# Kernel tuning notes

Measured on AMD Instinct MI355X. Metric: run time of the kernel, lower is better.

Reference implementation:

```python
import jax, jax.numpy as jnp
import numpy as np
import math

B, T, D, H, DFF = 4, 1024, 1024, 16, 4096
HD = D // H

def _c(a):
    # a: float array [2, ...] -> complex64 (a[0] real, a[1] imag)
    return jax.lax.complex(a[0], a[1])

def _clinear(z, W, b):
    # complex y = z @ W^T + b (torch nn.Linear convention)
    return z @ _c(W).T + _c(b)

def _cln(z, g, b, eps=1e-5):
    # per-component LayerNorm with separate affine for real/imag parts
    def ln(r):
        m = r.mean(-1, keepdims=True)
        v = ((r - m) ** 2).mean(-1, keepdims=True)
        return (r - m) / jnp.sqrt(v + eps)
    return jax.lax.complex(ln(z.real) * g[0] + b[0], ln(z.imag) * g[1] + b[1])

def _rope_phasor(t_len, dim):
    inv_freq = 1.0 / (10000.0 ** (jnp.arange(dim, dtype=jnp.float32) / dim))
    freqs = jnp.arange(t_len, dtype=jnp.float32)[:, None] * inv_freq[None, :]
    return jax.lax.complex(jnp.cos(freqs), jnp.sin(freqs))  # [T, HD]


def setup_inputs():
    key = jax.random.key(0)
    ks = iter(jax.random.split(key, 40))
    def p(shape, scale=0.02):
        return jax.random.normal(next(ks), shape, jnp.float32) * scale
    inp = {"x": p((2, B, T, D), 1.0), "mask": jnp.tril(jnp.ones((T, T), bool))}
    dims = {"wq": (D, D), "wk": (D, D), "wv": (D, D), "wo": (D, D),
            "wf1": (DFF, D), "wf2": (D, DFF), "wg": (D, D)}
    for name, (o, i) in dims.items():
        inp[name] = p((2, o, i))
        inp["b" + name[1:]] = p((2, o))
    inp["g1"] = jnp.ones((2, D), jnp.float32)
    inp["b1"] = jnp.zeros((2, D), jnp.float32)
    inp["g2"] = jnp.ones((2, D), jnp.float32)
    inp["b2"] = jnp.zeros((2, D), jnp.float32)
    return inp


def reference(x, mask, wq, bq, wk, bk, wv, bv, wo, bo,
              wf1, bf1, wf2, bf2, wg, bg, g1, b1, g2, b2):
    z = _c(x)  # [B,T,D] complex64
    ph = _rope_phasor(T, HD)[None, None]  # [1,1,T,HD]

    # ---- attention branch (pre-norm) ----
    nz = _cln(z, g1, b1)
    heads = lambda t: t.reshape(B, T, H, HD).transpose(0, 2, 1, 3)  # [B,H,T,HD]
    q = heads(_clinear(nz, wq, bq)) * ph
    k = heads(_clinear(nz, wk, bk)) * ph
    v = heads(_clinear(nz, wv, bv))
    score = jnp.einsum('bhqd,bhkd->bhqk', q, jnp.conj(k)) / math.sqrt(HD)
    mag = jnp.where(mask, jnp.abs(score), jnp.float32(-1e9))
    aw = jax.nn.softmax(mag, axis=-1)
    awc = jax.lax.complex(aw, jnp.zeros_like(aw))
    o = jnp.einsum('bhqk,bhkd->bhqd', awc, v)
    o = o.transpose(0, 2, 1, 3).reshape(B, T, D)
    z = z + _clinear(o, wo, bo)

    # ---- FFN branch with CReLU and AntiMatterGate ----
    nz = _cln(z, g2, b2)
    h = _clinear(nz, wf1, bf1)
    h = jax.lax.complex(jax.nn.relu(h.real), jax.nn.relu(h.imag))  # CReLU
    h = _clinear(h, wf2, bf2)
    g = _clinear(h, wg, bg)
    gn = jnp.abs(g) + 1e-8
    h = h * (g / jax.lax.complex(gn, jnp.zeros_like(gn)))  # phase-only gate
    z = z + h
    return jnp.stack([z.real, z.imag], axis=0)  # [2,B,T,D] float32
```

## Files before the change

### kernel.cpp

```cpp
#include <hip/hip_runtime.h>
#include <math.h>

#define B_ 4
#define T_ 1024
#define D_ 1024
#define H_ 16
#define DFF_ 4096
#define HD_ 64
#define BT_ (B_*T_)
#define PL ((size_t)BT_*D_)

typedef unsigned int uint;
typedef unsigned short ushort;
typedef __attribute__((ext_vector_type(8))) __bf16 bf16x8;
typedef __attribute__((ext_vector_type(4))) float f32x4;
typedef __attribute__((ext_vector_type(4))) uint uint4v;

__device__ __forceinline__ float b2f(ushort u){
  union{uint i; float f;} x; x.i = ((uint)u)<<16; return x.f;
}
__device__ __forceinline__ ushort f2b(float f){
  union{float f; uint i;} x; x.f = f;
  uint r = x.i + 0x7fffu + ((x.i>>16)&1u);
  return (ushort)(r>>16);
}
__device__ __forceinline__ void fsplit(float x, ushort& hi, ushort& lo){
  hi = f2b(x);
  lo = f2b(x - b2f(hi));
}
__device__ __forceinline__ bf16x8 negv(bf16x8 v){
  union{bf16x8 b; uint4v u;} t; t.b = v;
  t.u ^= 0x80008000u;
  return t.b;
}
__device__ __forceinline__ f32x4 mfma16(bf16x8 a, bf16x8 b, f32x4 c){
  return __builtin_amdgcn_mfma_f32_16x16x32_bf16(a,b,c,0,0,0);
}
__device__ __forceinline__ float block_sum(float v, float* sm){
  #pragma unroll
  for (int o=32;o>0;o>>=1) v += __shfl_down(v,o);
  int wid = threadIdx.x>>6;
  if ((threadIdx.x&63)==0) sm[wid]=v;
  __syncthreads();
  float r = sm[0]+sm[1]+sm[2]+sm[3];
  __syncthreads();
  return r;
}

__global__ __launch_bounds__(256) void cvt_split(const float* __restrict__ s,
                                                 ushort* __restrict__ d, long NK){
  long i = ((long)blockIdx.x*256 + threadIdx.x)*4;
  if (i >= NK) return;
  float4 vr = *(const float4*)(s+i);
  float4 vi = *(const float4*)(s+NK+i);
  ushort4 rh, rl, ih4, il4;
  fsplit(vr.x, rh.x, rl.x); fsplit(vr.y, rh.y, rl.y);
  fsplit(vr.z, rh.z, rl.z); fsplit(vr.w, rh.w, rl.w);
  fsplit(vi.x, ih4.x, il4.x); fsplit(vi.y, ih4.y, il4.y);
  fsplit(vi.z, ih4.z, il4.z); fsplit(vi.w, ih4.w, il4.w);
  *(ushort4*)(d + i)        = rh;
  *(ushort4*)(d + NK + i)   = rl;
  *(ushort4*)(d + 2*NK + i) = ih4;
  *(ushort4*)(d + 3*NK + i) = il4;
}

__global__ __launch_bounds__(256) void cln_kernel(const float* __restrict__ x,
    long PSx, int row0, const float* __restrict__ g, const float* __restrict__ bb,
    ushort* __restrict__ out, long PSo)
{
  __shared__ float sm[4];
  int row = blockIdx.x, comp = blockIdx.y;
  const float* xr = x + (size_t)comp*PSx + (size_t)(row0+row)*D_;
  float4 v = *(const float4*)(xr + threadIdx.x*4);
  float s = v.x+v.y+v.z+v.w;
  s = block_sum(s, sm);
  float mean = s * (1.0f/D_);
  float dx=v.x-mean, dy=v.y-mean, dz=v.z-mean, dw=v.w-mean;
  float s2 = dx*dx+dy*dy+dz*dz+dw*dw;
  s2 = block_sum(s2, sm);
  float inv = 1.0f/sqrtf(s2*(1.0f/D_) + 1e-5f);
  float4 gv = *(const float4*)(g + comp*D_ + threadIdx.x*4);
  float4 bv = *(const float4*)(bb + comp*D_ + threadIdx.x*4);
  float y0 = dx*inv*gv.x + bv.x, y1 = dy*inv*gv.y + bv.y;
  float y2 = dz*inv*gv.z + bv.z, y3 = dw*inv*gv.w + bv.w;
  ushort4 hh, ll;
  fsplit(y0, hh.x, ll.x); fsplit(y1, hh.y, ll.y);
  fsplit(y2, hh.z, ll.z); fsplit(y3, hh.w, ll.w);
  ushort* oh = out + (size_t)(comp*2)*PSo   + (size_t)row*D_;
  ushort* ol = out + (size_t)(comp*2+1)*PSo + (size_t)row*D_;
  *(ushort4*)(oh + threadIdx.x*4) = hh;
  *(ushort4*)(ol + threadIdx.x*4) = ll;
}

template<int BM,int BN,int WM,int WN,int NT>
__global__ __launch_bounds__(NT,1) void cgemm_split(
    const ushort* __restrict__ A, long PSa,
    const ushort* __restrict__ W, long PSw, long wstride,
    const float* b0, const float* b1, const float* b2,
    const float* __restrict__ Rr, const float* __restrict__ Ri,
    float* __restrict__ Cf, long PSc, long ostrideF,
    ushort* __restrict__ Cs, long PSs, long ostrideS,
    int M, int N, int K, int relu, int biasRow, int kslice)
{
  constexpr int NI = WM/16, NJ = WN/16;
  constexpr int NWX = BN/WN;
  constexpr int NPW = (BM+BN)*16/NT;
  constexpr int BUF = (BM+BN)*128;
  __shared__ __align__(16) ushort lds[2*BUF];
  const int tid = threadIdx.x, wave = tid>>6, lane = tid&63;
  const int quad = lane>>4, l16 = lane&15;
  const int lrow = lane>>3, sl = lane&7;

  const int gx = gridDim.x, gy = gridDim.y;
  const int nt = gx*gy;
  int lin = blockIdx.x + gx*blockIdx.y;
  int tile = (nt&7) ? lin : ((lin&7)*(nt>>3) + (lin>>3));
  int bxi, byi;
  if (gx <= gy){ bxi = tile % gx; byi = tile / gx; }
  else         { byi = tile % gy; bxi = tile / gy; }
  const int bm = byi*BM, bn = bxi*BN;

  const int gz = blockIdx.z;
  W += (size_t)gz*wstride;
  const float* bias = (gz==0)? b0 : (gz==1)? b1 : b2;
  if (Cf) Cf += (size_t)gz*ostrideF;
  if (Cs) Cs += (size_t)gz*ostrideS;
  const int wm = (wave/NWX)*WM, wn = (wave%NWX)*WN;
  const int kbeg = kslice ? gz*kslice : 0;
  const int kend = kslice ? kbeg+kslice : K;

  int sa[4];
  #pragma unroll
  for (int p=0;p<4;p++) sa[p] = (((p&1)<<2) + quad) ^ (l16&7);

  auto STAGE = [&](int bsel, int k0){
    #pragma unroll
    for (int n=0;n<NPW;n++){
      int it = wave*NPW + n;
      const ushort* mat; long PS; int brow, pair, r0, lbase;
      if (it < BM/4){
        pair = it/(BM/8); r0 = (it%(BM/8))*8;
        mat = A; PS = PSa; brow = bm;
        lbase = (pair*BM + r0)*8;
      } else {
        int itb = it - BM/4;
        pair = itb/(BN/8); r0 = (itb%(BN/8))*8;
        mat = W; PS = PSw; brow = bn;
        lbase = (2*BM + pair*BN + r0)*8;
      }
      int row = r0 + lrow;
      int s = sl ^ (row&7);
      int plane = pair*2 + (s>>2);
      const ushort* gp = mat + (size_t)plane*PS + (size_t)(brow+row)*K + k0 + (s&3)*8;
      __builtin_amdgcn_global_load_lds(
          (const __attribute__((address_space(1))) void*)gp,
          (__attribute__((address_space(3))) void*)&lds[bsel*BUF + lbase*8], 16, 0, 0);
    }
  };
  auto WAITN = [&](){
    if constexpr (NPW==16)      asm volatile("s_waitcnt vmcnt(16)" ::: "memory");
    else if constexpr (NPW==12) asm volatile("s_waitcnt vmcnt(12)" ::: "memory");
    else if constexpr (NPW==8)  asm volatile("s_waitcnt vmcnt(8)"  ::: "memory");
    else                        asm volatile("s_waitcnt vmcnt(0)"  ::: "memory");
  };
  auto WAIT0 = [&](){ asm volatile("s_waitcnt vmcnt(0)" ::: "memory"); };
  auto BAR = [&](){
    asm volatile("" ::: "memory");
    __builtin_amdgcn_s_barrier();
    asm volatile("" ::: "memory");
  };

  f32x4 accr[NI][NJ], acci[NI][NJ];
  #pragma unroll
  for (int i=0;i<NI;i++)
    #pragma unroll
    for (int j=0;j<NJ;j++){
      accr[i][j] = (f32x4){0.f,0.f,0.f,0.f};
      acci[i][j] = (f32x4){0.f,0.f,0.f,0.f};
    }

  int cur = 0;
  STAGE(0, kbeg);
  if (kbeg+32 < kend) STAGE(1, kbeg+32);
  for (int k0=kbeg; k0<kend; k0+=32){
    if (k0+32 < kend) WAITN(); else WAIT0();
    BAR();
    const int cb = cur*BUF;

    bf16x8 Bf[NJ][4];
    #pragma unroll
    for (int j=0;j<NJ;j++){
      int row = wn + j*16 + l16;
      #pragma unroll
      for (int p=0;p<4;p++)
        Bf[j][p] = *(const bf16x8*)&lds[cb + BM*128 + ((p>>1)*BN + row)*64 + sa[p]*8];
    }
    #pragma unroll
    for (int i=0;i<NI;i++){
      int row = wm + i*16 + l16;
      bf16x8 A0 = *(const bf16x8*)&lds[cb + (0*BM + row)*64 + sa[0]*8];
      bf16x8 A1 = *(const bf16x8*)&lds[cb + (0*BM + row)*64 + sa[1]*8];
      bf16x8 A2 = *(const bf16x8*)&lds[cb + (1*BM + row)*64 + sa[2]*8];
      bf16x8 A3 = *(const bf16x8*)&lds[cb + (1*BM + row)*64 + sa[3]*8];
      bf16x8 n2 = negv(A2), n3 = negv(A3);
      #pragma unroll
      for (int j=0;j<NJ;j++){
        f32x4 cr = accr[i][j], ci = acci[i][j];
        cr = mfma16(A0, Bf[j][0], cr); cr = mfma16(A0, Bf[j][1], cr); cr = mfma16(A1, Bf[j][0], cr);
        cr = mfma16(n2, Bf[j][2], cr); cr = mfma16(n2, Bf[j][3], cr); cr = mfma16(n3, Bf[j][2], cr);
        ci = mfma16(A0, Bf[j][2], ci); ci = mfma16(A0, Bf[j][3], ci); ci = mfma16(A1, Bf[j][2], ci);
        ci = mfma16(A2, Bf[j][0], ci); ci = mfma16(A2, Bf[j][1], ci); ci = mfma16(A3, Bf[j][0], ci);
        accr[i][j] = cr; acci[i][j] = ci;
      }
    }
    BAR();
    if (k0+64 < kend) STAGE(cur, k0+64);
    cur ^= 1;
  }
  #pragma unroll
  for (int i=0;i<NI;i++){
    #pragma unroll
    for (int j=0;j<NJ;j++){
      #pragma unroll
      for (int rg=0;rg<4;rg++){
        int row = bm + wm + i*16 + quad*4 + rg;
        int col = bn + wn + j*16 + l16;
        float br = 0.f, bi2 = 0.f;
        if (bias){
          br  = biasRow ? bias[row]   : bias[col];
          bi2 = biasRow ? bias[M+row] : bias[N+col];
        }
        float cr = accr[i][j][rg] + br;
        float ci = acci[i][j][rg] + bi2;
        size_t o = (size_t)row*N + col;
        if (Rr){ cr += Rr[o]; ci += Ri[o]; }
        if (relu){ cr = fmaxf(cr,0.f); ci = fmaxf(ci,0.f); }
        if (Cf){ Cf[o] = cr; Cf[PSc + o] = ci; }
        if (Cs){
          ushort h0,l0,h1v,l1;
          fsplit(cr,h0,l0); fsplit(ci,h1v,l1);
          Cs[o] = h0; Cs[PSs+o] = l0; Cs[2*PSs+o] = h1v; Cs[3*PSs+o] = l1;
        }
      }
    }
  }
}

__global__ __launch_bounds__(256) void rope_table(float* __restrict__ tab){
  int i = blockIdx.x*256 + threadIdx.x;
  int d = i & 63, t = i >> 6;
  float invf = expf(-(float)d * (9.210340371976184f/64.0f));
  float th = (float)t * invf;
  float s, c;
  sincosf(th, &s, &c);
  tab[2*i] = c; tab[2*i+1] = s;
}

__global__ __launch_bounds__(256) void rope_split(ushort* __restrict__ Q,
    ushort* __restrict__ Kk, const float* __restrict__ tab, long PS)
{
  size_t idx = (size_t)blockIdx.x*256 + threadIdx.x;
  int d = (int)(idx & (HD_-1));
  int t = (int)((idx >> 10) & (T_-1));
  float2 cs = *(const float2*)(tab + 2*(t*HD_ + d));
  float c = cs.x, s = cs.y;
  {
    float qr = b2f(Q[idx])      + b2f(Q[PS+idx]);
    float qi = b2f(Q[2*PS+idx]) + b2f(Q[3*PS+idx]);
    float nr = qr*c - qi*s, ni = qr*s + qi*c;
    ushort h,l;
    fsplit(nr,h,l); Q[idx]=h;      Q[PS+idx]=l;
    fsplit(ni,h,l); Q[2*PS+idx]=h; Q[3*PS+idx]=l;
  }
  {
    float kr = b2f(Kk[idx])      + b2f(Kk[PS+idx]);
    float ki = b2f(Kk[2*PS+idx]) + b2f(Kk[3*PS+idx]);
    float nr = kr*c - ki*s, ni = kr*s + ki*c;
    ushort h,l;
    fsplit(nr,h,l); Kk[idx]=h;      Kk[PS+idx]=l;
    fsplit(ni,h,l); Kk[2*PS+idx]=h; Kk[3*PS+idx]=l;
  }
}

__global__ __launch_bounds__(256) void attn_mfma(
    const ushort* __restrict__ Qg, const ushort* __restrict__ Kg,
    const ushort* __restrict__ Vt, long PS,
    ushort* __restrict__ O, long PSo)
{
  __shared__ __align__(16) ushort lds[24576];
  const int tid = threadIdx.x;
  const int wave = tid>>6, lane = tid&63;
  const int quad = lane>>4, l16 = lane&15;
  const int bh = blockIdx.x, b = bh>>4, h = bh&15;
  const int y = blockIdx.y;
  const int qb = (y<8) ? (15-y) : (y-8);
  const int qt0 = qb*64;
  const int qg = qt0 + wave*16 + l16;
  const int Pbase = 19456 + wave*1280;

  bf16x8 Qf[4][2];
  {
    size_t row = (size_t)(b*T_ + qt0 + wave*16 + l16);
    #pragma unroll
    for (int p=0;p<4;p++)
      #pragma unroll
      for (int dk=0;dk<2;dk++)
        Qf[p][dk] = *(const bf16x8*)(Qg + (size_t)p*PS + row*D_ + h*HD_ + dk*32 + quad*8);
  }
  f32x4 Or[4], Oi[4];
  #pragma unroll
  for (int dt=0;dt<4;dt++){ Or[dt]=(f32x4){0,0,0,0}; Oi[dt]=(f32x4){0,0,0,0}; }
  float mreg = -1e30f, lreg = 0.f;
  const int ntiles = 2*qb + 2;

  for (int tI=0; tI<ntiles; tI++){
    const int kt = tI*32;
    __syncthreads();
    #pragma unroll
    for (int r=0;r<4;r++){
      int id = r*256 + tid;
      int p = id>>8, rem = id&255;
      int row = rem>>3, slk = rem&7;
      const ushort* src = Kg + (size_t)p*PS + (size_t)(b*T_ + kt + row)*D_ + h*HD_ + slk*8;
      *(uint4*)&lds[p*2304 + row*72 + slk*8] = *(const uint4*)src;
    }
    {
      const ushort* srcp = Vt + (size_t)wave*PS + (size_t)(b*T_ + kt);
      #pragma unroll
      for (int r=0;r<4;r++){
        int chunk = r*64 + lane;
        int dd = chunk>>2, kg = chunk&3;
        *(uint4*)&lds[9216 + wave*2560 + dd*40 + kg*8] =
            *(const uint4*)(srcp + (size_t)(h*HD_ + dd)*BT_ + kg*8);
      }
    }
    __syncthreads();

    f32x4 sr[2], si[2];
    sr[0]=(f32x4){0,0,0,0}; sr[1]=(f32x4){0,0,0,0};
    si[0]=(f32x4){0,0,0,0}; si[1]=(f32x4){0,0,0,0};
    #pragma unroll
    for (int s=0;s<2;s++){
      #pragma unroll
      for (int dk=0;dk<2;dk++){
        int ra = (s*16+l16)*72 + dk*32 + quad*8;
        bf16x8 Krh = *(const bf16x8*)&lds[ra];
        bf16x8 Krl = *(const bf16x8*)&lds[2304 + ra];
        bf16x8 Kih = *(const bf16x8*)&lds[4608 + ra];
        bf16x8 Kil = *(const bf16x8*)&lds[6912 + ra];
        bf16x8 nKih = negv(Kih), nKil = negv(Kil);
        f32x4 r = sr[s], im = si[s];
        r = mfma16(Krh, Qf[0][dk], r); r = mfma16(Krh, Qf[1][dk], r); r = mfma16(Krl, Qf[0][dk], r);
        r = mfma16(Kih, Qf[2][dk], r); r = mfma16(Kih, Qf[3][dk], r); r = mfma16(Kil, Qf[2][dk], r);
        im = mfma16(Krh,  Qf[2][dk], im); im = mfma16(Krh,  Qf[3][dk], im); im = mfma16(Krl,  Qf[2][dk], im);
        im = mfma16(nKih, Qf[0][dk], im); im = mfma16(nKih, Qf[1][dk], im); im = mfma16(nKil, Qf[0][dk], im);
        sr[s]=r; si[s]=im;
      }
    }

    float pv[2][4];
    float mx = -1e30f;
    #pragma unroll
    for (int s=0;s<2;s++)
      #pragma unroll
      for (int rg=0;rg<4;rg++){
        float xr = sr[s][rg], xi = si[s][rg];
        float m = sqrtf(xr*xr + xi*xi)*0.125f;
        int kloc = kt + s*16 + quad*4 + rg;
        if (kloc > qg) m = -1e30f;
        pv[s][rg] = m;
        mx = fmaxf(mx, m);
      }
    mx = fmaxf(mx, __shfl_xor(mx,16));
    mx = fmaxf(mx, __shfl_xor(mx,32));
    float mnew = fmaxf(mreg, mx);
    float afac = __expf(mreg - mnew);
    float ps = 0.f;
    #pragma unroll
    for (int s=0;s<2;s++)
      #pragma unroll
      for (int rg=0;rg<4;rg++){
        float e = __expf(pv[s][rg] - mnew);
        pv[s][rg] = e; ps += e;
      }
    ps += __shfl_xor(ps,16); ps += __shfl_xor(ps,32);
    lreg = lreg*afac + ps;
    mreg = mnew;

    #pragma unroll
    for (int s=0;s<2;s++)
      #pragma unroll
      for (int rg=0;rg<4;rg++){
        ushort hi,lo; fsplit(pv[s][rg],hi,lo);
        int off = Pbase + l16*40 + s*16 + quad*4 + rg;
        lds[off] = hi; lds[off+640] = lo;
      }

    float af[4];
    #pragma unroll
    for (int rg=0;rg<4;rg++) af[rg] = __shfl(afac, quad*4+rg);
    #pragma unroll
    for (int dt=0;dt<4;dt++)
      #pragma unroll
      for (int rg=0;rg<4;rg++){ Or[dt][rg]*=af[rg]; Oi[dt][rg]*=af[rg]; }

    bf16x8 Ph  = *(const bf16x8*)&lds[Pbase +       l16*40 + quad*8];
    bf16x8 Plo = *(const bf16x8*)&lds[Pbase + 640 + l16*40 + quad*8];
    #pragma unroll
    for (int dt=0;dt<4;dt++){
      int rv = (dt*16+l16)*40 + quad*8;
      bf16x8 Vrh = *(const bf16x8*)&lds[9216 + rv];
      bf16x8 Vrl = *(const bf16x8*)&lds[9216 + 2560 + rv];
      bf16x8 Vih = *(const bf16x8*)&lds[9216 + 5120 + rv];
      bf16x8 Vil = *(const bf16x8*)&lds[9216 + 7680 + rv];
      f32x4 o_r = Or[dt], o_i = Oi[dt];
      o_r = mfma16(Ph, Vrh, o_r); o_r = mfma16(Ph, Vrl, o_r); o_r = mfma16(Plo, Vrh, o_r);
      o_i = mfma16(Ph, Vih, o_i); o_i = mfma16(Ph, Vil, o_i); o_i = mfma16(Plo, Vih, o_i);
      Or[dt]=o_r; Oi[dt]=o_i;
    }
  }

  float li[4];
  #pragma unroll
  for (int rg=0;rg<4;rg++) li[rg] = 1.0f / __shfl(lreg, quad*4+rg);
  #pragma unroll
  for (int dt=0;dt<4;dt++)
    #pragma unroll
    for (int rg=0;rg<4;rg++){
      float tr = Or[dt][rg]*li[rg], ti = Oi[dt][rg]*li[rg];
      ushort h0,l0,h1,l1;
      fsplit(tr,h0,l0); fsplit(ti,h1,l1);
      int rowt = qt0 + wave*16 + quad*4 + rg;
      size_t o = (size_t)(b*T_ + rowt)*D_ + h*HD_ + dt*16 + l16;
      O[o] = h0; O[PSo+o] = l0; O[2*PSo+o] = h1; O[3*PSo+o] = l1;
    }
}

__global__ __launch_bounds__(256) void hsum_kernel(const float* __restrict__ p0,
    const float* __restrict__ p1, ushort* __restrict__ out)
{
  size_t idx = (size_t)blockIdx.x*256 + threadIdx.x;
  const size_t M1s = (size_t)1<<20;
  float hr = p0[idx] + p1[idx];
  float hi = p0[M1s+idx] + p1[M1s+idx];
  ushort h0,l0,h1,l1;
  fsplit(hr,h0,l0); fsplit(hi,h1,l1);
  out[idx] = h0; out[M1s+idx] = l0; out[2*M1s+idx] = h1; out[3*M1s+idx] = l1;
}

__global__ __launch_bounds__(256) void gate_kernel(
    const float* __restrict__ z, const ushort* __restrict__ hB,
    const float* __restrict__ gp0, const float* __restrict__ gp1,
    float* __restrict__ out, int off)
{
  size_t idx = (size_t)blockIdx.x*256 + threadIdx.x;
  const size_t M1 = (size_t)1<<20;
  float hr = b2f(hB[idx])      + b2f(hB[M1+idx]);
  float hi = b2f(hB[2*M1+idx]) + b2f(hB[3*M1+idx]);
  float gr = gp0[idx] + gp1[idx];
  float gi = gp0[M1+idx] + gp1[M1+idx];
  float gn = sqrtf(gr*gr + gi*gi) + 1e-8f;
  float pr = (hr*gr - hi*gi) / gn;
  float pi = (hr*gi + hi*gr) / gn;
  size_t zoff = (size_t)off + idx;
  out[zoff]    = z[zoff] + pr;
  out[PL+zoff] = z[PL+zoff] + pi;
}

extern "C" void kernel_launch(void* const* d_in, const int* in_sizes, int n_in,
                              void* d_out, int out_size, void* d_ws, size_t ws_size,
                              hipStream_t stream)
{
  const float* x  = (const float*)d_in[0];
  const float* wq = (const float*)d_in[2];
  const float* bq = (const float*)d_in[3];
  const float* wk = (const float*)d_in[4];
  const float* bk = (const float*)d_in[5];
  const float* wv = (const float*)d_in[6];
  const float* bv = (const float*)d_in[7];
  const float* wo = (const float*)d_in[8];
  const float* bo = (const float*)d_in[9];
  const float* wf1= (const float*)d_in[10];
  const float* bf1= (const float*)d_in[11];
  const float* wf2= (const float*)d_in[12];
  const float* bf2= (const float*)d_in[13];
  const float* wg = (const float*)d_in[14];
  const float* bg = (const float*)d_in[15];
  const float* g1 = (const float*)d_in[16];
  const float* b1 = (const float*)d_in[17];
  const float* g2 = (const float*)d_in[18];
  const float* b2 = (const float*)d_in[19];
  float* out = (float*)d_out;
  char* w8 = (char*)d_ws;
  const size_t MB = (size_t)1<<20;
  const long M1 = 1L<<20, M4 = 1L<<22;

  ushort* wqkvB = (ushort*)(w8);
  ushort* woB   = (ushort*)(w8 + 24*MB);
  ushort* nzB   = (ushort*)(w8 + 32*MB);
  ushort* qS    = (ushort*)(w8 + 64*MB);
  ushort* kS    = (ushort*)(w8 + 96*MB);
  ushort* vtS   = (ushort*)(w8 + 128*MB);
  float*  ropeT = (float*)(w8 + 32*MB);
  ushort* oBc   = (ushort*)(w8 + 32*MB);
  float*  z     = (float*)(w8 + 64*MB);
  ushort* wf2B  = (ushort*)(w8);
  ushort* h1c   = (ushort*)(w8 + 32*MB);
  ushort* wf1B  = (ushort*)(w8 + 96*MB);
  ushort* wgB   = (ushort*)(w8 + 128*MB);
  ushort* nz2c  = (ushort*)(w8 + 136*MB);
  float*  p0F   = (float*)(w8 + 136*MB);
  ushort* hBc   = (ushort*)(w8 + 144*MB);
  float*  p1F   = (float*)(w8 + 152*MB);

  dim3 blk(256), blk5(512);
  cvt_split<<<1024, blk, 0, stream>>>(wq, wqkvB,        M1);
  cvt_split<<<1024, blk, 0, stream>>>(wk, wqkvB + 4*M1, M1);
  cvt_split<<<1024, blk, 0, stream>>>(wv, wqkvB + 8*M1, M1);
  cvt_split<<<1024, blk, 0, stream>>>(wo, woB,          M1);
  cln_kernel<<<dim3(BT_,2), blk, 0, stream>>>(x, (long)PL, 0, g1, b1, nzB, M4);
  cgemm_split<128,128,64,32,512><<<dim3(8,32,2), blk5, 0, stream>>>(
      nzB, M4, wqkvB, M1, 4*M1, bq, bk, nullptr,
      nullptr, nullptr, nullptr, 0, 0, qS, M4, 4*M4,
      4096, 1024, 1024, 0, 0, 0);
  cgemm_split<128,128,64,32,512><<<dim3(32,8,1), blk5, 0, stream>>>(
      wqkvB + 8*M1, M1, nzB, M4, 0, bv, nullptr, nullptr,
      nullptr, nullptr, nullptr, 0, 0, vtS, M4, 0,
      1024, 4096, 1024, 0, 1, 0);
  rope_table<<<256, blk, 0, stream>>>(ropeT);
  rope_split<<<16384, blk, 0, stream>>>(qS, kS, ropeT, M4);
  attn_mfma<<<dim3(64,16), blk, 0, stream>>>(qS, kS, vtS, M4, oBc, M4);
  cgemm_split<128,128,64,32,512><<<dim3(8,32,1), blk5, 0, stream>>>(
      oBc, M4, woB, M1, 0, bo, nullptr, nullptr,
      x, x + PL, z, (long)PL, 0, nullptr, 0, 0,
      4096, 1024, 1024, 0, 0, 0);
  cvt_split<<<4096, blk, 0, stream>>>(wf1, wf1B, M4);
  cvt_split<<<4096, blk, 0, stream>>>(wf2, wf2B, M4);
  cvt_split<<<1024, blk, 0, stream>>>(wg, wgB, M1);
  for (int c=0; c<4; c++){
    cln_kernel<<<dim3(1024,2), blk, 0, stream>>>(z, (long)PL, c*1024, g2, b2, nz2c, M1);
    cgemm_split<128,128,64,32,512><<<dim3(32,8,1), blk5, 0, stream>>>(
        nz2c, M1, wf1B, M4, 0, bf1, nullptr, nullptr,
        nullptr, nullptr, nullptr, 0, 0, h1c, M4, 0,
        1024, 4096, 1024, 1, 0, 0);
    cgemm_split<128,64,64,32,256><<<dim3(16,8,2), blk, 0, stream>>>(
        h1c, M4, wf2B, M4, 0, bf2, nullptr, nullptr,
        nullptr, nullptr, p0F, M1, M4, nullptr, 0, 0,
        1024, 1024, 4096, 0, 0, 2048);
    hsum_kernel<<<4096, blk, 0, stream>>>(p0F, p1F, hBc);
    cgemm_split<128,64,64,32,256><<<dim3(16,8,2), blk, 0, stream>>>(
        hBc, M1, wgB, M1, 0, bg, nullptr, nullptr,
        nullptr, nullptr, p0F, M1, M4, nullptr, 0, 0,
        1024, 1024, 1024, 0, 0, 512);
    gate_kernel<<<4096, blk, 0, stream>>>(z, hBc, p0F, p1F, out, c*(int)M1);
  }
}
```

Measured before the change: 1.787 ms.

## Add 32x32x16 MFMA complex GEMM kernel for the 128x128 GEMMs

Adds a new cgemm32 kernel that uses 32x32x16 bf16 MFMA instructions with 64x64 wave tiles and 256 threads, replacing the 512-thread 16x16 MFMA kernel for the QKV, V, output projection and FFN1 GEMMs. Larger MFMA tiles raise arithmetic intensity per LDS fragment load and cut instruction count. The new kernel loads straight from global memory into LDS with a 32-wide k-step and a single buffer, dropping the old double-buffered staging. That may expose load latency and raise register pressure from the larger accumulators.

```diff
diff --git a/kernel.cpp b/kernel.cpp
--- a/kernel.cpp
+++ b/kernel.cpp
@@ -14,6 +14,7 @@
 typedef unsigned short ushort;
 typedef __attribute__((ext_vector_type(8))) __bf16 bf16x8;
 typedef __attribute__((ext_vector_type(4))) float f32x4;
+typedef __attribute__((ext_vector_type(16))) float f32x16;
 typedef __attribute__((ext_vector_type(4))) uint uint4v;
 
 __device__ __forceinline__ float b2f(ushort u){
@@ -35,6 +36,9 @@
 }
 __device__ __forceinline__ f32x4 mfma16(bf16x8 a, bf16x8 b, f32x4 c){
   return __builtin_amdgcn_mfma_f32_16x16x32_bf16(a,b,c,0,0,0);
+}
+__device__ __forceinline__ f32x16 mfma32(bf16x8 a, bf16x8 b, f32x16 c){
+  return __builtin_amdgcn_mfma_f32_32x32x16_bf16(a,b,c,0,0,0);
 }
 __device__ __forceinline__ float block_sum(float v, float* sm){
   #pragma unroll
@@ -225,6 +229,142 @@
       for (int rg=0;rg<4;rg++){
         int row = bm + wm + i*16 + quad*4 + rg;
         int col = bn + wn + j*16 + l16;
+        float br = 0.f, bi2 = 0.f;
+        if (bias){
+          br  = biasRow ? bias[row]   : bias[col];
+          bi2 = biasRow ? bias[M+row] : bias[N+col];
+        }
+        float cr = accr[i][j][rg] + br;
+        float ci = acci[i][j][rg] + bi2;
+        size_t o = (size_t)row*N + col;
+        if (Rr){ cr += Rr[o]; ci += Ri[o]; }
+        if (relu){ cr = fmaxf(cr,0.f); ci = fmaxf(ci,0.f); }
+        if (Cf){ Cf[o] = cr; Cf[PSc + o] = ci; }
+        if (Cs){
+          ushort h0,l0,h1v,l1;
+          fsplit(cr,h0,l0); fsplit(ci,h1v,l1);
+          Cs[o] = h0; Cs[PSs+o] = l0; Cs[2*PSs+o] = h1v; Cs[3*PSs+o] = l1;
+        }
+      }
+    }
+  }
+}
+
+template<int BM,int BN,int WM,int WN,int NT>
+__global__ __launch_bounds__(NT,2) void cgemm32(
+    const ushort* __restrict__ A, long PSa,
+    const ushort* __restrict__ W, long PSw, long wstride,
+    const float* b0, const float* b1, const float* b2,
+    const float* __restrict__ Rr, const float* __restrict__ Ri,
+    float* __restrict__ Cf, long PSc, long ostrideF,
+    ushort* __restrict__ Cs, long PSs, long ostrideS,
+    int M, int N, int K, int relu, int biasRow, int kslice)
+{
+  constexpr int NI = WM/32, NJ = WN/32;
+  constexpr int NWX = BN/WN;
+  constexpr int NPW = (BM+BN)*16/NT;
+  __shared__ __align__(16) ushort lds[(BM+BN)*128];
+  const int tid = threadIdx.x, wave = tid>>6, lane = tid&63;
+  const int l31 = lane&31, half = lane>>5, e7 = lane&7;
+  const int lrow = lane>>3, sl = lane&7;
+
+  const int gx = gridDim.x, gy = gridDim.y;
+  const int nt = gx*gy;
+  int lin = blockIdx.x + gx*blockIdx.y;
+  int tile = (nt&7) ? lin : ((lin&7)*(nt>>3) + (lin>>3));
+  int bxi, byi;
+  if (gx <= gy){ bxi = tile % gx; byi = tile / gx; }
+  else         { byi = tile % gy; bxi = tile / gy; }
+  const int bm = byi*BM, bn = bxi*BN;
+
+  const int gz = blockIdx.z;
+  W += (size_t)gz*wstride;
+  const float* bias = (gz==0)? b0 : (gz==1)? b1 : b2;
+  if (Cf) Cf += (size_t)gz*ostrideF;
+  if (Cs) Cs += (size_t)gz*ostrideS;
+  const int wm = (wave/NWX)*WM, wn = (wave%NWX)*WN;
+  const int kbeg = kslice ? gz*kslice : 0;
+  const int kend = kslice ? kbeg+kslice : K;
+
+  int sa[4][2];
+  #pragma unroll
+  for (int p=0;p<4;p++)
+    #pragma unroll
+    for (int kh=0;kh<2;kh++)
+      sa[p][kh] = (((p&1)<<2) + kh*2 + half) ^ e7;
+
+  f32x16 accr[NI][NJ], acci[NI][NJ];
+  #pragma unroll
+  for (int i=0;i<NI;i++)
+    #pragma unroll
+    for (int j=0;j<NJ;j++)
+      #pragma unroll
+      for (int r=0;r<16;r++){ accr[i][j][r]=0.f; acci[i][j][r]=0.f; }
+
+  for (int k0=kbeg; k0<kend; k0+=32){
+    __syncthreads();
+    #pragma unroll
+    for (int n=0;n<NPW;n++){
+      int it = wave*NPW + n;
+      const ushort* mat; long PS; int brow, pair, r0, lbase;
+      if (it < BM/4){
+        pair = it/(BM/8); r0 = (it%(BM/8))*8;
+        mat = A; PS = PSa; brow = bm;
+        lbase = (pair*BM + r0)*8;
+      } else {
+        int itb = it - BM/4;
+        pair = itb/(BN/8); r0 = (itb%(BN/8))*8;
+        mat = W; PS = PSw; brow = bn;
+        lbase = (2*BM + pair*BN + r0)*8;
+      }
+      int row = r0 + lrow;
+      int s = sl ^ (row&7);
+      int plane = pair*2 + (s>>2);
+      const ushort* gp = mat + (size_t)plane*PS + (size_t)(brow+row)*K + k0 + (s&3)*8;
+      __builtin_amdgcn_global_load_lds(
+          (const __attribute__((address_space(1))) void*)gp,
+          (__attribute__((address_space(3))) void*)&lds[lbase*8], 16, 0, 0);
+    }
+    __syncthreads();
+
+    #pragma unroll
+    for (int kh=0;kh<2;kh++){
+      bf16x8 Bf[NJ][4];
+      #pragma unroll
+      for (int j=0;j<NJ;j++){
+        int row = wn + j*32 + l31;
+        #pragma unroll
+        for (int p=0;p<4;p++)
+          Bf[j][p] = *(const bf16x8*)&lds[(2*BM + (p>>1)*BN + row)*64 + sa[p][kh]*8];
+      }
+      #pragma unroll
+      for (int i=0;i<NI;i++){
+        int row = wm + i*32 + l31;
+        bf16x8 A0 = *(const bf16x8*)&lds[(0*BM + row)*64 + sa[0][kh]*8];
+        bf16x8 A1 = *(const bf16x8*)&lds[(0*BM + row)*64 + sa[1][kh]*8];
+        bf16x8 A2 = *(const bf16x8*)&lds[(1*BM + row)*64 + sa[2][kh]*8];
+        bf16x8 A3 = *(const bf16x8*)&lds[(1*BM + row)*64 + sa[3][kh]*8];
+        bf16x8 n2 = negv(A2), n3 = negv(A3);
+        #pragma unroll
+        for (int j=0;j<NJ;j++){
+          f32x16 cr = accr[i][j], ci = acci[i][j];
+          cr = mfma32(A0, Bf[j][0], cr); cr = mfma32(A0, Bf[j][1], cr); cr = mfma32(A1, Bf[j][0], cr);
+          cr = mfma32(n2, Bf[j][2], cr); cr = mfma32(n2, Bf[j][3], cr); cr = mfma32(n3, Bf[j][2], cr);
+          ci = mfma32(A0, Bf[j][2], ci); ci = mfma32(A0, Bf[j][3], ci); ci = mfma32(A1, Bf[j][2], ci);
+          ci = mfma32(A2, Bf[j][0], ci); ci = mfma32(A2, Bf[j][1], ci); ci = mfma32(A3, Bf[j][0], ci);
+          accr[i][j] = cr; acci[i][j] = ci;
+        }
+      }
+    }
+  }
+  #pragma unroll
+  for (int i=0;i<NI;i++){
+    #pragma unroll
+    for (int j=0;j<NJ;j++){
+      #pragma unroll
+      for (int rg=0;rg<16;rg++){
+        int row = bm + wm + i*32 + (rg&3) + 8*(rg>>2) + 4*half;
+        int col = bn + wn + j*32 + l31;
         float br = 0.f, bi2 = 0.f;
         if (bias){
           br  = biasRow ? bias[row]   : bias[col];
@@ -513,24 +653,24 @@
   ushort* hBc   = (ushort*)(w8 + 144*MB);
   float*  p1F   = (float*)(w8 + 152*MB);
 
-  dim3 blk(256), blk5(512);
+  dim3 blk(256);
   cvt_split<<<1024, blk, 0, stream>>>(wq, wqkvB,        M1);
   cvt_split<<<1024, blk, 0, stream>>>(wk, wqkvB + 4*M1, M1);
   cvt_split<<<1024, blk, 0, stream>>>(wv, wqkvB + 8*M1, M1);
   cvt_split<<<1024, blk, 0, stream>>>(wo, woB,          M1);
   cln_kernel<<<dim3(BT_,2), blk, 0, stream>>>(x, (long)PL, 0, g1, b1, nzB, M4);
-  cgemm_split<128,128,64,32,512><<<dim3(8,32,2), blk5, 0, stream>>>(
+  cgemm32<128,128,64,64,256><<<dim3(8,32,2), blk, 0, stream>>>(
       nzB, M4, wqkvB, M1, 4*M1, bq, bk, nullptr,
       nullptr, nullptr, nullptr, 0, 0, qS, M4, 4*M4,
       4096, 1024, 1024, 0, 0, 0);
-  cgemm_split<128,128,64,32,512><<<dim3(32,8,1), blk5, 0, stream>>>(
+  cgemm32<128,128,64,64,256><<<dim3(32,8,1), blk, 0, stream>>>(
       wqkvB + 8*M1, M1, nzB, M4, 0, bv, nullptr, nullptr,
       nullptr, nullptr, nullptr, 0, 0, vtS, M4, 0,
       1024, 4096, 1024, 0, 1, 0);
   rope_table<<<256, blk, 0, stream>>>(ropeT);
   rope_split<<<16384, blk, 0, stream>>>(qS, kS, ropeT, M4);
   attn_mfma<<<dim3(64,16), blk, 0, stream>>>(qS, kS, vtS, M4, oBc, M4);
-  cgemm_split<128,128,64,32,512><<<dim3(8,32,1), blk5, 0, stream>>>(
+  cgemm32<128,128,64,64,256><<<dim3(8,32,1), blk, 0, stream>>>(
       oBc, M4, woB, M1, 0, bo, nullptr, nullptr,
       x, x + PL, z, (long)PL, 0, nullptr, 0, 0,
       4096, 1024, 1024, 0, 0, 0);
@@ -539,7 +679,7 @@
   cvt_split<<<1024, blk, 0, stream>>>(wg, wgB, M1);
   for (int c=0; c<4; c++){
     cln_kernel<<<dim3(1024,2), blk, 0, stream>>>(z, (long)PL, c*1024, g2, b2, nz2c, M1);
-    cgemm_split<128,128,64,32,512><<<dim3(32,8,1), blk5, 0, stream>>>(
+    cgemm32<128,128,64,64,256><<<dim3(32,8,1), blk, 0, stream>>>(
         nz2c, M1, wf1B, M4, 0, bf1, nullptr, nullptr,
         nullptr, nullptr, nullptr, 0, 0, h1c, M4, 0,
         1024, 4096, 1024, 1, 0, 0);
```

Result: slower. 2.051 ms (+14.8%).
